# Kernel tuning notes

Hardware: AMD Instinct MI355X
Metric: run time of the kernel (lower is better)

## Reference

```python
import jax, jax.numpy as jnp
import numpy as np

D = 512       # embed_dim
H = 8         # num_heads
HD = D // H   # head_dim = 64
B = 16
TQ = 512      # query length (current segment)
TK = 1024     # key length (memory + current)
GRU_BIAS = 2.0


def _layer_norm(x, g, b, eps=1e-5):
    mu = jnp.mean(x, axis=-1, keepdims=True)
    var = jnp.mean((x - mu) ** 2, axis=-1, keepdims=True)
    return (x - mu) * jax.lax.rsqrt(var + eps) * g + b


def _gelu(x):
    # torch nn.GELU() default is the exact erf form
    return jax.nn.gelu(x, approximate=False)


def _rel_shift(x):
    # Transformer-XL relative shift. x: [B, H, Tq, Tk]
    b, h, tq, tk = x.shape
    x = jnp.pad(x, ((0, 0), (0, 0), (0, 0), (1, 0)))
    x = x.reshape(b, h, tk + 1, tq)[:, :, 1:, :]
    return x.reshape(b, h, tq, tk)


def _gru_gate(x, y, W, bg):
    # GTrXL gating: x is the residual stream, y the sublayer output.
    Wr, Ur, Wz, Uz, Wg, Ug = W
    r = jax.nn.sigmoid(y @ Wr + x @ Ur)
    z = jax.nn.sigmoid(y @ Wz + x @ Uz - bg)
    h = jnp.tanh(y @ Wg + (r * x) @ Ug)
    return (1.0 - z) * x + z * h


def setup_inputs() -> dict:
    key = jax.random.key(0)
    ks = jax.random.split(key, 16)
    s = 0.02
    return {
        "query": jax.random.normal(ks[0], (B, TQ, D), jnp.float32),
        "key": jax.random.normal(ks[1], (B, TK, D), jnp.float32),
        "pos_embedding": jax.random.normal(ks[2], (TK, D), jnp.float32),
        "U": jax.random.normal(ks[3], (H, HD), jnp.float32) * s,
        "V": jax.random.normal(ks[4], (H, HD), jnp.float32) * s,
        # attention projections: Wq, Wk, Wv, Wpos, Wout (no biases)
        "attn_W": jax.random.normal(ks[5], (5, D, D), jnp.float32) * s,
        "ln1_g": jnp.ones((D,), jnp.float32),
        "ln1_b": jnp.zeros((D,), jnp.float32),
        "ln2_g": jnp.ones((D,), jnp.float32),
        "ln2_b": jnp.zeros((D,), jnp.float32),
        # GRU gates: stacked [Wr, Ur, Wz, Uz, Wg, Ug], bias bg init to gru_bias
        "gate1_W": jax.random.normal(ks[6], (6, D, D), jnp.float32) * s,
        "gate1_b": jnp.full((D,), GRU_BIAS, jnp.float32),
        "gate2_W": jax.random.normal(ks[7], (6, D, D), jnp.float32) * s,
        "gate2_b": jnp.full((D,), GRU_BIAS, jnp.float32),
        "fc_W1": jax.random.normal(ks[8], (D, 4 * D), jnp.float32) * s,
        "fc_b1": jnp.zeros((4 * D,), jnp.float32),
        "fc_W2": jax.random.normal(ks[9], (4 * D, D), jnp.float32) * s,
        "fc_b2": jnp.zeros((D,), jnp.float32),
    }


def reference(query, key, pos_embedding, U, V, attn_W,
              ln1_g, ln1_b, ln2_g, ln2_b,
              gate1_W, gate1_b, gate2_W, gate2_b,
              fc_W1, fc_b1, fc_W2, fc_b2):
    b, tq, d = query.shape
    tk = key.shape[1]
    hd = d // H

    nq = _layer_norm(query, ln1_g, ln1_b)
    nk = _layer_norm(key, ln1_g, ln1_b)

    Wq, Wk, Wv, Wp, Wo = attn_W
    q = (nq @ Wq).reshape(b, tq, H, hd)
    k = (nk @ Wk).reshape(b, tk, H, hd)
    v = (nk @ Wv).reshape(b, tk, H, hd)
    p = (pos_embedding @ Wp).reshape(tk, H, hd)

    # Transformer-XL: content score (q+U)k^T + position score (q+V)p^T (rel-shifted)
    AC = jnp.einsum('bqhd,bkhd->bhqk', q + U, k)
    BD = _rel_shift(jnp.einsum('bqhd,khd->bhqk', q + V, p))
    scores = (AC + BD) / jnp.sqrt(jnp.asarray(hd, query.dtype))
    attn = jax.nn.softmax(scores, axis=-1)

    Y = jnp.einsum('bhqk,bkhd->bqhd', attn, v).reshape(b, tq, d) @ Wo
    Y = _gelu(Y)  # dropout = 0.0

    out = _gru_gate(query, Y, gate1_W, gate1_b)
    h2 = _layer_norm(out, ln2_g, ln2_b)
    E = _gelu(_gelu(h2 @ fc_W1 + fc_b1) @ fc_W2 + fc_b2)
    out = _gru_gate(out, E, gate2_W, gate2_b)
    return out
```

## Files before the change

kernel.cpp:

```cpp
#include <hip/hip_runtime.h>
#include <hip/hip_bf16.h>

typedef unsigned short u16;
typedef __attribute__((ext_vector_type(4))) float f4;
typedef __attribute__((ext_vector_type(8))) short s16x8;
typedef __attribute__((ext_vector_type(8))) unsigned short u16x8;
typedef __attribute__((ext_vector_type(4))) unsigned short u16x4;
typedef __attribute__((ext_vector_type(4))) int i32x4;
typedef __attribute__((ext_vector_type(2))) unsigned u32x2;

__device__ __forceinline__ u16 f2bf(float x){
  unsigned u = __float_as_uint(x);
  u += 0x7fffu + ((u >> 16) & 1u);
  return (u16)(u >> 16);
}
__device__ __forceinline__ float bf2f(u16 h){ return __uint_as_float(((unsigned)h) << 16); }

__device__ __forceinline__ unsigned cvt_pk_bf16(float lo, float hi){
  unsigned r;
  asm("v_cvt_pk_bf16_f32 %0, %1, %2" : "=v"(r) : "v"(lo), "v"(hi));
  return r;
}

__device__ __forceinline__ void gload_lds16(const u16* g, u16* l){
  __builtin_amdgcn_global_load_lds((__attribute__((address_space(1))) void*)g,
                                   (__attribute__((address_space(3))) void*)l, 16, 0, 0);
}

__device__ __forceinline__ float gelu_f(float x){
  float u = x * (0.7978845608f + 0.0356774081f * x * x);
  float e = __expf(-2.f * u);
  return x * __builtin_amdgcn_rcpf(1.f + e);
}
__device__ __forceinline__ float sig_f(float x){
  float e = __expf(-x);
  return __builtin_amdgcn_rcpf(1.f + e);
}
__device__ __forceinline__ float tanh_f(float x){
  float e = __expf(-2.f * fabsf(x));
  float t = (1.f - e) * __builtin_amdgcn_rcpf(1.f + e);
  return copysignf(t, x);
}

struct GemmP {
  const u16* A; const u16* B;
  const u16* A2; const u16* B2;
  int K1, K2, lda, ldb, H;
  long long sAb, sAh, sBb, sBh;
  u16* C; long long sCb, sCh; int ldc;
  u16* C2;
  const float* bias; const float* bias2;
  u16* S;
};

enum { EPI_BF16=0, EPI_QUV=1, EPI_SIG=2, EPI_TANH=3, EPI_GELU=4, EPI_BD=5 };

template<int BM, int BN, int EPI, int DB>
__launch_bounds__(256)
__global__ void gemm_k(GemmP p) {
  constexpr int WN = (BN >= 128) ? 2 : 1;
  constexpr int WM = 4 / WN;
  constexpr int TM = BM / WM, TN = BN / WN;
  constexpr int FM = TM / 16, FN = TN / 16;
  constexpr int BUFE = (BM + BN) * 64;

  __shared__ __align__(16) u16 lds[BUFE * (DB ? 2 : 1)];

  const int tid = threadIdx.x;
  const int w = tid >> 6, lane = tid & 63;
  const int bz = blockIdx.z;
  const int b = bz / p.H, h = bz - b * p.H;
  const int m0 = blockIdx.x * BM, n0 = blockIdx.y * BN;

  const u16* Ab0 = p.A + (long long)b * p.sAb + (long long)h * p.sAh + (long long)m0 * p.lda;
  const u16* Bb0 = p.B + (long long)b * p.sBb + (long long)h * p.sBh + (long long)n0 * p.ldb;
  const u16* Ab1 = p.A2 ? p.A2 + (long long)m0 * p.lda : (const u16*)0;
  const u16* Bb1 = p.B2 ? p.B2 + (long long)n0 * p.ldb : (const u16*)0;

  f4 acc[FM][FN];
  #pragma unroll
  for (int i = 0; i < FM; ++i)
    #pragma unroll
    for (int j = 0; j < FN; ++j) acc[i][j] = f4{0.f, 0.f, 0.f, 0.f};

  const int s1 = p.K1 >> 6;
  const int st = s1 + (p.K2 >> 6);
  const int wM = w / WN, wN = w - wM * WN;

  const int srow = tid >> 3;
  const long long sc8 = (long long)(((tid & 7) ^ (srow & 7)) << 3);
  const long long aoff = (long long)srow * p.lda + sc8;
  const long long boff = (long long)srow * p.ldb + sc8;

  auto stage = [&](int s, u16* lA_, u16* lB_) {
    const u16* Ab; const u16* Bb; int k0;
    if (s < s1) { Ab = Ab0; Bb = Bb0; k0 = s << 6; }
    else        { Ab = Ab1; Bb = Bb1; k0 = (s - s1) << 6; }
    const u16* pa = Ab + aoff + k0;
    const u16* pb = Bb + boff + k0;
    #pragma unroll
    for (int i = 0; i < (BM >> 5); ++i)
      gload_lds16(pa + (long long)(i * 32) * p.lda, lA_ + (size_t)(i * 4 + w) * 512);
    #pragma unroll
    for (int i = 0; i < (BN >> 5); ++i)
      gload_lds16(pb + (long long)(i * 32) * p.ldb, lB_ + (size_t)(i * 4 + w) * 512);
  };

  auto compute = [&](const u16* lA_, const u16* lB_) {
    #pragma unroll
    for (int kk = 0; kk < 2; ++kk) {
      const int kb = lane >> 4;
      const int gc = kk * 4 + kb;
      s16x8 av[FM], bv[FN];
      #pragma unroll
      for (int fm = 0; fm < FM; ++fm) {
        int r = wM * TM + fm * 16 + (lane & 15);
        av[fm] = *(const s16x8*)(lA_ + r * 64 + ((gc ^ (r & 7)) << 3));
      }
      #pragma unroll
      for (int fn = 0; fn < FN; ++fn) {
        int r = wN * TN + fn * 16 + (lane & 15);
        bv[fn] = *(const s16x8*)(lB_ + r * 64 + ((gc ^ (r & 7)) << 3));
      }
      #pragma unroll
      for (int fm = 0; fm < FM; ++fm)
        #pragma unroll
        for (int fn = 0; fn < FN; ++fn)
          acc[fm][fn] = __builtin_amdgcn_mfma_f32_16x16x32_bf16(av[fm], bv[fn], acc[fm][fn], 0, 0, 0);
    }
  };

  if constexpr (DB) {
    stage(0, lds, lds + BM * 64);
    __syncthreads();
    for (int s = 0; s < st; ++s) {
      u16* cur = lds + (size_t)(s & 1) * BUFE;
      if (s + 1 < st) {
        u16* nxt = lds + (size_t)((s + 1) & 1) * BUFE;
        stage(s + 1, nxt, nxt + BM * 64);
      }
      compute(cur, cur + BM * 64);
      __syncthreads();
    }
  } else {
    for (int s = 0; s < st; ++s) {
      stage(s, lds, lds + BM * 64);
      __syncthreads();
      compute(lds, lds + BM * 64);
      __syncthreads();
    }
  }

  const int rb = (lane >> 4) << 2;
  const int cb = lane & 15;

  if constexpr (EPI == EPI_BD) {
    #pragma unroll
    for (int fm = 0; fm < FM; ++fm)
      #pragma unroll
      for (int fn = 0; fn < FN; ++fn)
        #pragma unroll
        for (int r = 0; r < 4; ++r) {
          int row = m0 + wM * TM + fm * 16 + rb + r;
          int t   = n0 + wN * TN + fn * 16 + cb;
          int bb = row >> 9, q = row & 511;
          u16* Sp = p.S + (size_t)(bb * 8 + h) * 524800;
          Sp[(size_t)q * 1025 + 1 + t] = f2bf(acc[fm][fn][r] * 0.125f);
          if (t == 0 && q > 0) Sp[(size_t)q * 1025] = 0;
        }
  } else if constexpr (EPI == EPI_QUV) {
    #pragma unroll
    for (int fm = 0; fm < FM; ++fm)
      #pragma unroll
      for (int fn = 0; fn < FN; ++fn)
        #pragma unroll
        for (int r = 0; r < 4; ++r) {
          int row = m0 + wM * TM + fm * 16 + rb + r;
          int col = n0 + wN * TN + fn * 16 + cb;
          size_t o = (size_t)row * p.ldc + col;
          float x = acc[fm][fn][r];
          p.C[o]  = f2bf(x + p.bias[col]);
          p.C2[o] = f2bf(x + p.bias2[col]);
        }
  } else {
    u16* Cb = p.C + (long long)b * p.sCb + (long long)h * p.sCh;
    #pragma unroll
    for (int fm = 0; fm < FM; ++fm)
      #pragma unroll
      for (int fn = 0; fn < FN; ++fn)
        #pragma unroll
        for (int r = 0; r < 4; ++r) {
          int row = m0 + wM * TM + fm * 16 + rb + r;
          int col = n0 + wN * TN + fn * 16 + cb;
          float x = acc[fm][fn][r];
          if (p.bias) x += p.bias[col];
          if constexpr (EPI == EPI_SIG)  x = sig_f(x);
          if constexpr (EPI == EPI_TANH) x = tanh_f(x);
          if constexpr (EPI == EPI_GELU) x = gelu_f(x);
          Cb[(size_t)row * p.ldc + col] = f2bf(x);
        }
  }
}

__launch_bounds__(512)
__global__ void fattn_k(const u16* __restrict__ qU, const u16* __restrict__ kv,
                        const u16* __restrict__ vT, const u16* __restrict__ BD,
                        u16* __restrict__ Y) {
  __shared__ __align__(16) u16 sBuf[2 * 16384];

  const int tid = threadIdx.x, w = tid >> 6, lane = tid & 63;
  const int q0 = blockIdx.x * 128;
  const int bz = blockIdx.y, b = bz >> 3, h = bz & 7;
  const int cq = lane & 15, kb = lane >> 4;
  const u16* Sb = BD + (size_t)bz * 524800;

  auto stage = [&](int j0, u16* buf) {
    u16* sK_ = buf; u16* sV_ = buf + 4096; u16* sB_ = buf + 8192;
    {
      int c = tid, row = c >> 3, cc = c & 7, sc = cc ^ (row & 7);
      gload_lds16(kv + ((size_t)(b * 1024 + j0 + row)) * 1024 + h * 64 + sc * 8,
                  sK_ + (size_t)w * 512);
      gload_lds16(vT + (size_t)bz * 65536 + (size_t)row * 1024 + j0 + sc * 8,
                  sV_ + (size_t)w * 512);
    }
    #pragma unroll
    for (int i = 0; i < 2; ++i) {
      int c = i * 512 + tid, row = c >> 3, cc = c & 7, sc = cc ^ (row & 7);
      gload_lds16(Sb + 512 + (size_t)(q0 + row) * 1024 + j0 + sc * 8,
                  sB_ + (size_t)(i * 8 + w) * 512);
    }
  };

  const int qloc = w * 16 + cq;
  const u16* qrow = qU + ((size_t)(b * 512 + q0 + qloc)) * 512 + h * 64;
  s16x8 qb0 = *(const s16x8*)(qrow + kb * 8);
  s16x8 qb1 = *(const s16x8*)(qrow + 32 + kb * 8);

  stage(0, sBuf);
  __syncthreads();

  float m_s = -1e30f, l_s = 0.f;
  f4 O[4];
  #pragma unroll
  for (int fd = 0; fd < 4; ++fd) O[fd] = f4{0.f, 0.f, 0.f, 0.f};

  const int sw = qloc & 7;
  const int idxA = (cq + ((kb & 1) * 2) * 16) * 4;
  const int idxB = idxA + 64;

  for (int it = 0; it < 16; ++it) {
    u16* buf = sBuf + (size_t)(it & 1) * 16384;
    u16* sK_ = buf; u16* sV_ = buf + 4096; u16* sB_ = buf + 8192;
    if (it < 15) stage((it + 1) * 64, sBuf + (size_t)((it + 1) & 1) * 16384);

    f4 acc[4];
    #pragma unroll
    for (int fkv = 0; fkv < 4; ++fkv) acc[fkv] = f4{0.f, 0.f, 0.f, 0.f};
    #pragma unroll
    for (int fkv = 0; fkv < 4; ++fkv) {
      int r = fkv * 16 + cq;
      s16x8 a0 = *(const s16x8*)(sK_ + r * 64 + ((kb ^ (r & 7)) << 3));
      s16x8 a1 = *(const s16x8*)(sK_ + r * 64 + (((4 + kb) ^ (r & 7)) << 3));
      acc[fkv] = __builtin_amdgcn_mfma_f32_16x16x32_bf16(a0, qb0, acc[fkv], 0, 0, 0);
      acc[fkv] = __builtin_amdgcn_mfma_f32_16x16x32_bf16(a1, qb1, acc[fkv], 0, 0, 0);
    }

    float p[4][4];
    float tm = -1e30f;
    #pragma unroll
    for (int fkv = 0; fkv < 4; ++fkv) {
      int j8 = 2 * fkv + (kb >> 1);
      u16x4 bdv = *(const u16x4*)(sB_ + qloc * 64 + ((j8 ^ sw) << 3) + (kb & 1) * 4);
      #pragma unroll
      for (int r = 0; r < 4; ++r) {
        float s = acc[fkv][r] * 0.125f + bf2f(bdv[r]);
        p[fkv][r] = s;
        tm = fmaxf(tm, s);
      }
    }
    tm = fmaxf(tm, __shfl_xor(tm, 16));
    tm = fmaxf(tm, __shfl_xor(tm, 32));
    float mn = fmaxf(m_s, tm);
    float al = __expf(m_s - mn);
    m_s = mn;
    float ps = 0.f;
    #pragma unroll
    for (int fkv = 0; fkv < 4; ++fkv)
      #pragma unroll
      for (int r = 0; r < 4; ++r) { p[fkv][r] = __expf(p[fkv][r] - mn); ps += p[fkv][r]; }
    ps += __shfl_xor(ps, 16);
    ps += __shfl_xor(ps, 32);
    l_s = l_s * al + ps;
    #pragma unroll
    for (int fd = 0; fd < 4; ++fd)
      #pragma unroll
      for (int r = 0; r < 4; ++r) O[fd][r] *= al;

    unsigned W[4][2];
    #pragma unroll
    for (int fkv = 0; fkv < 4; ++fkv) {
      W[fkv][0] = cvt_pk_bf16(p[fkv][0], p[fkv][1]);
      W[fkv][1] = cvt_pk_bf16(p[fkv][2], p[fkv][3]);
    }
    s16x8 pb[2];
    #pragma unroll
    for (int c = 0; c < 2; ++c) {
      int a00 = __builtin_amdgcn_ds_bpermute(idxA, (int)W[2 * c][0]);
      int a01 = __builtin_amdgcn_ds_bpermute(idxA, (int)W[2 * c][1]);
      int a10 = __builtin_amdgcn_ds_bpermute(idxA, (int)W[2 * c + 1][0]);
      int a11 = __builtin_amdgcn_ds_bpermute(idxA, (int)W[2 * c + 1][1]);
      int b00 = __builtin_amdgcn_ds_bpermute(idxB, (int)W[2 * c][0]);
      int b01 = __builtin_amdgcn_ds_bpermute(idxB, (int)W[2 * c][1]);
      int b10 = __builtin_amdgcn_ds_bpermute(idxB, (int)W[2 * c + 1][0]);
      int b11 = __builtin_amdgcn_ds_bpermute(idxB, (int)W[2 * c + 1][1]);
      bool hi = (kb >= 2);
      i32x4 t;
      t[0] = hi ? a10 : a00;
      t[1] = hi ? a11 : a01;
      t[2] = hi ? b10 : b00;
      t[3] = hi ? b11 : b01;
      pb[c] = *(s16x8*)&t;
    }

    #pragma unroll
    for (int c = 0; c < 2; ++c)
      #pragma unroll
      for (int fd = 0; fd < 4; ++fd) {
        int rd = fd * 16 + cq;
        s16x8 vb = *(const s16x8*)(sV_ + rd * 64 + (((c * 4 + kb) ^ (rd & 7)) << 3));
        O[fd] = __builtin_amdgcn_mfma_f32_16x16x32_bf16(vb, pb[c], O[fd], 0, 0, 0);
      }
    __syncthreads();
  }

  float invl = 1.f / l_s;
  u16* yrow = Y + ((size_t)(b * 512 + q0 + qloc)) * 512 + h * 64;
  #pragma unroll
  for (int fd = 0; fd < 4; ++fd) {
    unsigned w0 = cvt_pk_bf16(O[fd][0] * invl, O[fd][1] * invl);
    unsigned w1 = cvt_pk_bf16(O[fd][2] * invl, O[fd][3] * invl);
    u32x2 st; st[0] = w0; st[1] = w1;
    *(u32x2*)(yrow + fd * 16 + kb * 4) = st;
  }
}

__launch_bounds__(256)
__global__ void ln_k(const float* __restrict__ x, const float* __restrict__ g,
                     const float* __restrict__ be, u16* __restrict__ out) {
  int row  = blockIdx.x * 4 + (threadIdx.x >> 6);
  int lane = threadIdx.x & 63;
  const float* xr = x + (size_t)row * 512 + lane * 8;
  f4 v0 = *(const f4*)xr;
  f4 v1 = *(const f4*)(xr + 4);
  float s = 0.f, q = 0.f;
  #pragma unroll
  for (int i = 0; i < 4; ++i) { s += v0[i] + v1[i]; q += v0[i]*v0[i] + v1[i]*v1[i]; }
  #pragma unroll
  for (int o = 32; o > 0; o >>= 1) { s += __shfl_xor(s, o); q += __shfl_xor(q, o); }
  float mu = s * (1.f / 512.f);
  float rs = rsqrtf(q * (1.f / 512.f) - mu * mu + 1e-5f);
  int c = lane * 8;
  u16x8 o;
  #pragma unroll
  for (int i = 0; i < 8; ++i) {
    float xx = (i < 4) ? v0[i] : v1[i - 4];
    o[i] = f2bf((xx - mu) * rs * g[c + i] + be[c + i]);
  }
  *(u16x8*)(out + (size_t)row * 512 + c) = o;
}

__device__ __forceinline__ void tbody(float (*t)[65], const float* src, u16* dst,
                                      int R, int C, int bx, int by, int tid) {
  int c0 = bx * 64, r0 = by * 64;
  #pragma unroll
  for (int i = 0; i < 4; ++i) {
    int r = i * 16 + (tid >> 4);
    int c4 = (tid & 15) * 4;
    f4 v = *(const f4*)(src + (size_t)(r0 + r) * C + c0 + c4);
    t[r][c4] = v.x; t[r][c4 + 1] = v.y; t[r][c4 + 2] = v.z; t[r][c4 + 3] = v.w;
  }
  __syncthreads();
  #pragma unroll
  for (int i = 0; i < 2; ++i) {
    int id = i * 256 + tid;
    int rr = id >> 3, c8 = (id & 7) * 8;
    u16x8 o;
    #pragma unroll
    for (int j = 0; j < 8; ++j) o[j] = f2bf(t[c8 + j][rr]);
    *(u16x8*)(dst + (size_t)(c0 + rr) * R + r0 + c8) = o;
  }
}

__launch_bounds__(256)
__global__ void tsq_k(const float* aW, const float* g1W, const float* g2W, u16* wT) {
  __shared__ float t[64][65];
  int z = blockIdx.z;
  const int lut[6] = {0, 2, 1, 3, 4, 5};
  const float* src; u16* dst;
  if (z < 5)       { src = aW  + (size_t)z * 262144;        dst = wT + (size_t)z * 262144; }
  else if (z < 11) { int j = z - 5;  src = g1W + (size_t)j * 262144; dst = wT + (size_t)(5 + lut[j]) * 262144; }
  else             { int j = z - 11; src = g2W + (size_t)j * 262144; dst = wT + (size_t)(11 + lut[j]) * 262144; }
  tbody(t, src, dst, 512, 512, blockIdx.x, blockIdx.y, threadIdx.x);
}

__launch_bounds__(256)
__global__ void tgen_k(const float* src, u16* dst, int R, int C) {
  __shared__ float t[64][65];
  tbody(t, src, dst, R, C, blockIdx.x, blockIdx.y, threadIdx.x);
}

__launch_bounds__(256)
__global__ void vtrans_k(const u16* kv, u16* vT) {
  int jt = blockIdx.x, h = blockIdx.y, b = blockIdx.z;
  __shared__ u16 t[64][72];
  int tid = threadIdx.x;
  const u16* src = kv + ((size_t)b * 1024 + jt * 64) * 1024 + 512 + h * 64;
  #pragma unroll
  for (int i = 0; i < 2; ++i) {
    int id = i * 256 + tid;
    int r = id >> 3, c = (id & 7) * 8;
    u16x8 v = *(const u16x8*)(src + (size_t)r * 1024 + c);
    #pragma unroll
    for (int j = 0; j < 8; ++j) t[r][c + j] = v[j];
  }
  __syncthreads();
  u16* dst = vT + (size_t)(b * 8 + h) * 65536 + (size_t)jt * 64;
  #pragma unroll
  for (int i = 0; i < 2; ++i) {
    int id = i * 256 + tid;
    int d = id >> 3, c = (id & 7) * 8;
    u16x8 o;
    #pragma unroll
    for (int j = 0; j < 8; ++j) o[j] = t[c + j][d];
    *(u16x8*)(dst + (size_t)d * 1024 + c) = o;
  }
}

__launch_bounds__(256)
__global__ void conv_k(const float* in, u16* out, int n8) {
  int i = blockIdx.x * 256 + threadIdx.x;
  if (i >= n8) return;
  const float* p = in + (size_t)i * 8;
  f4 a = *(const f4*)p, b = *(const f4*)(p + 4);
  u16x8 o;
  #pragma unroll
  for (int j = 0; j < 4; ++j) { o[j] = f2bf(a[j]); o[4 + j] = f2bf(b[j]); }
  *(u16x8*)(out + (size_t)i * 8) = o;
}

__launch_bounds__(256)
__global__ void bias_k(const float* g1b, const float* g2b, float* b1, float* b2) {
  int i = blockIdx.x * 256 + threadIdx.x;
  if (i < 1024) { b1[i] = (i < 512) ? 0.f : -g1b[i - 512]; b2[i] = (i < 512) ? 0.f : -g2b[i - 512]; }
}

__launch_bounds__(256)
__global__ void rx_k(const u16* rz, const float* x, u16* rx) {
  int i = blockIdx.x * 256 + threadIdx.x;
  int m = i >> 6, d8 = (i & 63) << 3;
  u16x8 rv = *(const u16x8*)(rz + (size_t)m * 1024 + d8);
  const float* xp = x + (size_t)m * 512 + d8;
  f4 x0 = *(const f4*)xp, x1 = *(const f4*)(xp + 4);
  u16x8 o;
  #pragma unroll
  for (int j = 0; j < 4; ++j) { o[j] = f2bf(bf2f(rv[j]) * x0[j]); o[4 + j] = f2bf(bf2f(rv[4 + j]) * x1[j]); }
  *(u16x8*)(rx + (size_t)m * 512 + d8) = o;
}

__launch_bounds__(256)
__global__ void comb_k(const u16* rz, const u16* hg, const float* x, float* of, u16* ob) {
  int i = blockIdx.x * 256 + threadIdx.x;
  int m = i >> 6, d8 = (i & 63) << 3;
  u16x8 zv = *(const u16x8*)(rz + (size_t)m * 1024 + 512 + d8);
  u16x8 hv = *(const u16x8*)(hg + (size_t)m * 512 + d8);
  const float* xp = x + (size_t)m * 512 + d8;
  f4 x0 = *(const f4*)xp, x1 = *(const f4*)(xp + 4);
  f4 o0, o1; u16x8 obv;
  #pragma unroll
  for (int j = 0; j < 4; ++j) {
    float z = bf2f(zv[j]), hh = bf2f(hv[j]);
    float r = (1.f - z) * x0[j] + z * hh; o0[j] = r; obv[j] = f2bf(r);
  }
  #pragma unroll
  for (int j = 0; j < 4; ++j) {
    float z = bf2f(zv[4 + j]), hh = bf2f(hv[4 + j]);
    float r = (1.f - z) * x1[j] + z * hh; o1[j] = r; obv[4 + j] = f2bf(r);
  }
  float* op = of + (size_t)m * 512 + d8;
  *(f4*)op = o0; *(f4*)(op + 4) = o1;
  if (ob) *(u16x8*)(ob + (size_t)m * 512 + d8) = obv;
}

extern "C" void kernel_launch(void* const* d_in, const int* in_sizes, int n_in,
                              void* d_out, int out_size, void* d_ws, size_t ws_size,
                              hipStream_t stream) {
  const float* query = (const float*)d_in[0];
  const float* key   = (const float*)d_in[1];
  const float* pos   = (const float*)d_in[2];
  const float* U     = (const float*)d_in[3];
  const float* V     = (const float*)d_in[4];
  const float* attnW = (const float*)d_in[5];
  const float* ln1g  = (const float*)d_in[6];
  const float* ln1b  = (const float*)d_in[7];
  const float* ln2g  = (const float*)d_in[8];
  const float* ln2b  = (const float*)d_in[9];
  const float* g1W   = (const float*)d_in[10];
  const float* g1b   = (const float*)d_in[11];
  const float* g2W   = (const float*)d_in[12];
  const float* g2b   = (const float*)d_in[13];
  const float* fcW1  = (const float*)d_in[14];
  const float* fcb1  = (const float*)d_in[15];
  const float* fcW2  = (const float*)d_in[16];
  const float* fcb2  = (const float*)d_in[17];
  float* outp = (float*)d_out;

  char* base = (char*)d_ws;
  size_t off = 0;
  auto alloc = [&](size_t bytes) -> char* {
    char* p = base + off;
    off += (bytes + 255) & ~(size_t)255;
    return p;
  };

  u16* wT     = (u16*)alloc(17ull * 262144 * 2);
  u16* fc1T   = (u16*)alloc(2048ull * 512 * 2);
  u16* fc2T   = (u16*)alloc(2048ull * 512 * 2);
  u16* posb   = (u16*)alloc(1024ull * 512 * 2);
  u16* pbf    = (u16*)alloc(1024ull * 512 * 2);
  float* bias1 = (float*)alloc(1024 * 4);
  float* bias2 = (float*)alloc(1024 * 4);
  u16* nq     = (u16*)alloc(8192ull * 512 * 2);
  u16* nk     = (u16*)alloc(16384ull * 512 * 2);
  u16* xq     = (u16*)alloc(8192ull * 512 * 2);
  u16* qU     = (u16*)alloc(8192ull * 512 * 2);
  u16* qV     = (u16*)alloc(8192ull * 512 * 2);
  u16* kv     = (u16*)alloc(16384ull * 1024 * 2);
  u16* y1     = (u16*)alloc(8192ull * 512 * 2);
  u16* ob1    = (u16*)alloc(8192ull * 512 * 2);
  u16* S      = (u16*)alloc(128ull * 524800 * 2 + 4096);
  if (off > ws_size) return;

  u16* Y = nq;
  u16* vT = nk;
  float* out1f = (float*)qU;
  u16* rz1 = S;
  u16* rx1 = S + 8388608;
  u16* hg1 = rx1 + 4194304;
  u16* h2  = hg1 + 4194304;
  u16* e1  = h2 + 4194304;
  u16* y2  = e1 + 16777216;
  u16* rz2 = y2 + 4194304;
  u16* rx2 = rz2 + 8388608;
  u16* hg2 = rx2 + 4194304;

  bias_k<<<dim3(4), dim3(256), 0, stream>>>(g1b, g2b, bias1, bias2);
  tsq_k<<<dim3(8, 8, 17), dim3(256), 0, stream>>>(attnW, g1W, g2W, wT);
  tgen_k<<<dim3(32, 8), dim3(256), 0, stream>>>(fcW1, fc1T, 512, 2048);
  tgen_k<<<dim3(8, 32), dim3(256), 0, stream>>>(fcW2, fc2T, 2048, 512);
  conv_k<<<dim3(256), dim3(256), 0, stream>>>(pos, posb, 65536);
  conv_k<<<dim3(2048), dim3(256), 0, stream>>>(query, xq, 524288);
  ln_k<<<dim3(2048), dim3(256), 0, stream>>>(query, ln1g, ln1b, nq);
  ln_k<<<dim3(4096), dim3(256), 0, stream>>>(key, ln1g, ln1b, nk);

  { GemmP p{}; p.A = nq; p.B = wT; p.K1 = 512; p.lda = 512; p.ldb = 512; p.H = 1;
    p.C = qU; p.C2 = qV; p.ldc = 512; p.bias = U; p.bias2 = V;
    gemm_k<64,128,EPI_QUV,1><<<dim3(128,4,1), dim3(256), 0, stream>>>(p); }
  { GemmP p{}; p.A = nk; p.B = wT + 1ull*262144; p.K1 = 512; p.lda = 512; p.ldb = 512; p.H = 1;
    p.C = kv; p.ldc = 1024;
    gemm_k<64,128,EPI_BF16,1><<<dim3(256,8,1), dim3(256), 0, stream>>>(p); }
  { GemmP p{}; p.A = posb; p.B = wT + 3ull*262144; p.K1 = 512; p.lda = 512; p.ldb = 512; p.H = 1;
    p.C = pbf; p.ldc = 512;
    gemm_k<64,128,EPI_BF16,1><<<dim3(16,4,1), dim3(256), 0, stream>>>(p); }
  vtrans_k<<<dim3(16, 8, 16), dim3(256), 0, stream>>>(kv, vT);

  { GemmP p{}; p.A = qV; p.lda = 512; p.sAh = 64;
    p.B = pbf; p.ldb = 512; p.sBh = 64; p.K1 = 64; p.H = 8; p.S = S;
    gemm_k<128,128,EPI_BD,0><<<dim3(64,8,8), dim3(256), 0, stream>>>(p); }

  fattn_k<<<dim3(4, 128), dim3(512), 0, stream>>>(qU, kv, vT, S, Y);

  { GemmP p{}; p.A = Y; p.B = wT + 4ull*262144; p.K1 = 512; p.lda = 512; p.ldb = 512; p.H = 1;
    p.C = y1; p.ldc = 512;
    gemm_k<64,128,EPI_GELU,1><<<dim3(128,4,1), dim3(256), 0, stream>>>(p); }

  { GemmP p{}; p.A = y1; p.B = wT + 5ull*262144; p.K1 = 512;
    p.A2 = xq; p.B2 = wT + 7ull*262144; p.K2 = 512;
    p.lda = 512; p.ldb = 512; p.H = 1; p.C = rz1; p.ldc = 1024; p.bias = bias1;
    gemm_k<64,128,EPI_SIG,1><<<dim3(128,8,1), dim3(256), 0, stream>>>(p); }
  rx_k<<<dim3(2048), dim3(256), 0, stream>>>(rz1, query, rx1);
  { GemmP p{}; p.A = y1; p.B = wT + 9ull*262144; p.K1 = 512;
    p.A2 = rx1; p.B2 = wT + 10ull*262144; p.K2 = 512;
    p.lda = 512; p.ldb = 512; p.H = 1; p.C = hg1; p.ldc = 512;
    gemm_k<64,128,EPI_TANH,1><<<dim3(128,4,1), dim3(256), 0, stream>>>(p); }
  comb_k<<<dim3(2048), dim3(256), 0, stream>>>(rz1, hg1, query, out1f, ob1);

  ln_k<<<dim3(2048), dim3(256), 0, stream>>>(out1f, ln2g, ln2b, h2);
  { GemmP p{}; p.A = h2; p.B = fc1T; p.K1 = 512; p.lda = 512; p.ldb = 512; p.H = 1;
    p.C = e1; p.ldc = 2048; p.bias = fcb1;
    gemm_k<64,128,EPI_GELU,1><<<dim3(128,16,1), dim3(256), 0, stream>>>(p); }
  { GemmP p{}; p.A = e1; p.B = fc2T; p.K1 = 2048; p.lda = 2048; p.ldb = 2048; p.H = 1;
    p.C = y2; p.ldc = 512; p.bias = fcb2;
    gemm_k<64,128,EPI_GELU,1><<<dim3(128,4,1), dim3(256), 0, stream>>>(p); }

  { GemmP p{}; p.A = y2; p.B = wT + 11ull*262144; p.K1 = 512;
    p.A2 = ob1; p.B2 = wT + 13ull*262144; p.K2 = 512;
    p.lda = 512; p.ldb = 512; p.H = 1; p.C = rz2; p.ldc = 1024; p.bias = bias2;
    gemm_k<64,128,EPI_SIG,1><<<dim3(128,8,1), dim3(256), 0, stream>>>(p); }
  rx_k<<<dim3(2048), dim3(256), 0, stream>>>(rz2, out1f, rx2);
  { GemmP p{}; p.A = y2; p.B = wT + 15ull*262144; p.K1 = 512;
    p.A2 = rx2; p.B2 = wT + 16ull*262144; p.K2 = 512;
    p.lda = 512; p.ldb = 512; p.H = 1; p.C = hg2; p.ldc = 512;
    gemm_k<64,128,EPI_TANH,1><<<dim3(128,4,1), dim3(256), 0, stream>>>(p); }
  comb_k<<<dim3(2048), dim3(256), 0, stream>>>(rz2, hg2, out1f, outp, (u16*)nullptr);
}
```

Before: 400.3 us.

## Fuse V transpose into KV projection epilogue and triple-buffer attention loads

The K/V projection GEMM now writes K in row-major form and V already transposed per head, so the separate vtrans kernel and its extra pass over V go away. The flash attention kernel now triple-buffers K/V tiles and double-buffers the BD tiles. It waits with explicit vmcnt counts and a raw barrier instead of a full __syncthreads, so loads stay in flight across iterations. The FC1 GEMM switches to a new three-buffer prefetch mode. The cost is more LDS per block, which may lower occupancy, and hand-written waitcnt logic that must match the exact number of loads issued.

New measurement: 424.5 us. 6.0% more time.

```diff
diff --git a/kernel.cpp b/kernel.cpp
--- a/kernel.cpp
+++ b/kernel.cpp
@@ -26,6 +26,10 @@
   __builtin_amdgcn_global_load_lds((__attribute__((address_space(1))) void*)g,
                                    (__attribute__((address_space(3))) void*)l, 16, 0, 0);
 }
+
+__device__ __forceinline__ void vm_wait0(){ asm volatile("s_waitcnt vmcnt(0)" ::: "memory"); }
+__device__ __forceinline__ void vm_wait2(){ asm volatile("s_waitcnt vmcnt(2)" ::: "memory"); }
+__device__ __forceinline__ void vm_wait6(){ asm volatile("s_waitcnt vmcnt(6)" ::: "memory"); }
 
 __device__ __forceinline__ float gelu_f(float x){
   float u = x * (0.7978845608f + 0.0356774081f * x * x);
@@ -53,7 +57,7 @@
   u16* S;
 };
 
-enum { EPI_BF16=0, EPI_QUV=1, EPI_SIG=2, EPI_TANH=3, EPI_GELU=4, EPI_BD=5 };
+enum { EPI_BF16=0, EPI_QUV=1, EPI_SIG=2, EPI_TANH=3, EPI_GELU=4, EPI_BD=5, EPI_KVT=6 };
 
 template<int BM, int BN, int EPI, int DB>
 __launch_bounds__(256)
@@ -63,8 +67,9 @@
   constexpr int TM = BM / WM, TN = BN / WN;
   constexpr int FM = TM / 16, FN = TN / 16;
   constexpr int BUFE = (BM + BN) * 64;
-
-  __shared__ __align__(16) u16 lds[BUFE * (DB ? 2 : 1)];
+  constexpr int NBUF = (DB == 2) ? 3 : (DB == 1) ? 2 : 1;
+
+  __shared__ __align__(16) u16 lds[BUFE * NBUF];
 
   const int tid = threadIdx.x;
   const int w = tid >> 6, lane = tid & 63;
@@ -130,7 +135,21 @@
     }
   };
 
-  if constexpr (DB) {
+  if constexpr (DB == 2) {
+    stage(0, lds, lds + BM * 64);
+    stage(1, lds + BUFE, lds + BUFE + BM * 64);
+    for (int s = 0; s < st; ++s) {
+      if (s + 1 < st) vm_wait6(); else vm_wait0();
+      __builtin_amdgcn_s_barrier();
+      __builtin_amdgcn_sched_barrier(0);
+      u16* cur = lds + (size_t)(s % 3) * BUFE;
+      if (s + 2 < st) {
+        u16* nxt = lds + (size_t)((s + 2) % 3) * BUFE;
+        stage(s + 2, nxt, nxt + BM * 64);
+      }
+      compute(cur, cur + BM * 64);
+    }
+  } else if constexpr (DB == 1) {
     stage(0, lds, lds + BM * 64);
     __syncthreads();
     for (int s = 0; s < st; ++s) {
@@ -168,6 +187,32 @@
           Sp[(size_t)q * 1025 + 1 + t] = f2bf(acc[fm][fn][r] * 0.125f);
           if (t == 0 && q > 0) Sp[(size_t)q * 1025] = 0;
         }
+  } else if constexpr (EPI == EPI_KVT) {
+    if (n0 < 512) {
+      #pragma unroll
+      for (int fm = 0; fm < FM; ++fm)
+        #pragma unroll
+        for (int fn = 0; fn < FN; ++fn)
+          #pragma unroll
+          for (int r = 0; r < 4; ++r) {
+            int row = m0 + wM * TM + fm * 16 + rb + r;
+            int col = n0 + wN * TN + fn * 16 + cb;
+            p.C[(size_t)row * 512 + col] = f2bf(acc[fm][fn][r]);
+          }
+    } else {
+      #pragma unroll
+      for (int fm = 0; fm < FM; ++fm)
+        #pragma unroll
+        for (int fn = 0; fn < FN; ++fn) {
+          int j0r = m0 + wM * TM + fm * 16 + rb;
+          int d   = n0 - 512 + wN * TN + fn * 16 + cb;
+          int bb = j0r >> 10, j = j0r & 1023;
+          u16x4 v;
+          #pragma unroll
+          for (int r = 0; r < 4; ++r) v[r] = f2bf(acc[fm][fn][r]);
+          *(u16x4*)(p.C2 + (((size_t)(bb * 8 + (d >> 6))) << 16) + (size_t)(d & 63) * 1024 + j) = v;
+        }
+    }
   } else if constexpr (EPI == EPI_QUV) {
     #pragma unroll
     for (int fm = 0; fm < FM; ++fm)
@@ -203,10 +248,10 @@
 }
 
 __launch_bounds__(512)
-__global__ void fattn_k(const u16* __restrict__ qU, const u16* __restrict__ kv,
+__global__ void fattn_k(const u16* __restrict__ qU, const u16* __restrict__ kvK,
                         const u16* __restrict__ vT, const u16* __restrict__ BD,
                         u16* __restrict__ Y) {
-  __shared__ __align__(16) u16 sBuf[2 * 16384];
+  __shared__ __align__(16) u16 sBuf[3 * 8192 + 2 * 8192];
 
   const int tid = threadIdx.x, w = tid >> 6, lane = tid & 63;
   const int q0 = blockIdx.x * 128;
@@ -214,20 +259,19 @@
   const int cq = lane & 15, kb = lane >> 4;
   const u16* Sb = BD + (size_t)bz * 524800;
 
-  auto stage = [&](int j0, u16* buf) {
-    u16* sK_ = buf; u16* sV_ = buf + 4096; u16* sB_ = buf + 8192;
-    {
-      int c = tid, row = c >> 3, cc = c & 7, sc = cc ^ (row & 7);
-      gload_lds16(kv + ((size_t)(b * 1024 + j0 + row)) * 1024 + h * 64 + sc * 8,
-                  sK_ + (size_t)w * 512);
-      gload_lds16(vT + (size_t)bz * 65536 + (size_t)row * 1024 + j0 + sc * 8,
-                  sV_ + (size_t)w * 512);
-    }
+  auto stageKV = [&](int j0, u16* buf) {
+    int row = tid >> 3, sc = (tid & 7) ^ (row & 7);
+    gload_lds16(kvK + ((size_t)(b * 1024 + j0 + row)) * 512 + h * 64 + sc * 8,
+                buf + (size_t)w * 512);
+    gload_lds16(vT + (size_t)bz * 65536 + (size_t)row * 1024 + j0 + sc * 8,
+                buf + 4096 + (size_t)w * 512);
+  };
+  auto stageBD = [&](int j0, u16* buf) {
     #pragma unroll
     for (int i = 0; i < 2; ++i) {
-      int c = i * 512 + tid, row = c >> 3, cc = c & 7, sc = cc ^ (row & 7);
+      int c = i * 512 + tid, row = c >> 3, sc = (c & 7) ^ (row & 7);
       gload_lds16(Sb + 512 + (size_t)(q0 + row) * 1024 + j0 + sc * 8,
-                  sB_ + (size_t)(i * 8 + w) * 512);
+                  buf + (size_t)(i * 8 + w) * 512);
     }
   };
 
@@ -236,8 +280,9 @@
   s16x8 qb0 = *(const s16x8*)(qrow + kb * 8);
   s16x8 qb1 = *(const s16x8*)(qrow + 32 + kb * 8);
 
-  stage(0, sBuf);
-  __syncthreads();
+  stageKV(0, sBuf);
+  stageBD(0, sBuf + 24576);
+  stageKV(64, sBuf + 8192);
 
   float m_s = -1e30f, l_s = 0.f;
   f4 O[4];
@@ -249,9 +294,16 @@
   const int idxB = idxA + 64;
 
   for (int it = 0; it < 16; ++it) {
-    u16* buf = sBuf + (size_t)(it & 1) * 16384;
-    u16* sK_ = buf; u16* sV_ = buf + 4096; u16* sB_ = buf + 8192;
-    if (it < 15) stage((it + 1) * 64, sBuf + (size_t)((it + 1) & 1) * 16384);
+    if (it < 15) vm_wait2(); else vm_wait0();
+    __builtin_amdgcn_s_barrier();
+    __builtin_amdgcn_sched_barrier(0);
+
+    u16* kvb = sBuf + (size_t)(it % 3) * 8192;
+    u16* sK_ = kvb; u16* sV_ = kvb + 4096;
+    u16* sB_ = sBuf + 24576 + (size_t)(it & 1) * 8192;
+
+    if (it + 1 < 16) stageBD((it + 1) * 64, sBuf + 24576 + (size_t)((it + 1) & 1) * 8192);
+    if (it + 2 < 16) stageKV((it + 2) * 64, sBuf + (size_t)((it + 2) % 3) * 8192);
 
     f4 acc[4];
     #pragma unroll
@@ -330,7 +382,6 @@
         s16x8 vb = *(const s16x8*)(sV_ + rd * 64 + (((c * 4 + kb) ^ (rd & 7)) << 3));
         O[fd] = __builtin_amdgcn_mfma_f32_16x16x32_bf16(vb, pb[c], O[fd], 0, 0, 0);
       }
-    __syncthreads();
   }
 
   float invl = 1.f / l_s;
@@ -407,33 +458,6 @@
 __global__ void tgen_k(const float* src, u16* dst, int R, int C) {
   __shared__ float t[64][65];
   tbody(t, src, dst, R, C, blockIdx.x, blockIdx.y, threadIdx.x);
-}
-
-__launch_bounds__(256)
-__global__ void vtrans_k(const u16* kv, u16* vT) {
-  int jt = blockIdx.x, h = blockIdx.y, b = blockIdx.z;
-  __shared__ u16 t[64][72];
-  int tid = threadIdx.x;
-  const u16* src = kv + ((size_t)b * 1024 + jt * 64) * 1024 + 512 + h * 64;
-  #pragma unroll
-  for (int i = 0; i < 2; ++i) {
-    int id = i * 256 + tid;
-    int r = id >> 3, c = (id & 7) * 8;
-    u16x8 v = *(const u16x8*)(src + (size_t)r * 1024 + c);
-    #pragma unroll
-    for (int j = 0; j < 8; ++j) t[r][c + j] = v[j];
-  }
-  __syncthreads();
-  u16* dst = vT + (size_t)(b * 8 + h) * 65536 + (size_t)jt * 64;
-  #pragma unroll
-  for (int i = 0; i < 2; ++i) {
-    int id = i * 256 + tid;
-    int d = id >> 3, c = (id & 7) * 8;
-    u16x8 o;
-    #pragma unroll
-    for (int j = 0; j < 8; ++j) o[j] = t[c + j][d];
-    *(u16x8*)(dst + (size_t)d * 1024 + c) = o;
-  }
 }
 
 __launch_bounds__(256)
@@ -534,14 +558,14 @@
   u16* xq     = (u16*)alloc(8192ull * 512 * 2);
   u16* qU     = (u16*)alloc(8192ull * 512 * 2);
   u16* qV     = (u16*)alloc(8192ull * 512 * 2);
-  u16* kv     = (u16*)alloc(16384ull * 1024 * 2);
+  u16* kvK    = (u16*)alloc(16384ull * 512 * 2);
+  u16* vT     = (u16*)alloc(128ull * 65536 * 2);
   u16* y1     = (u16*)alloc(8192ull * 512 * 2);
   u16* ob1    = (u16*)alloc(8192ull * 512 * 2);
   u16* S      = (u16*)alloc(128ull * 524800 * 2 + 4096);
   if (off > ws_size) return;
 
   u16* Y = nq;
-  u16* vT = nk;
   float* out1f = (float*)qU;
   u16* rz1 = S;
   u16* rx1 = S + 8388608;
@@ -566,18 +590,17 @@
     p.C = qU; p.C2 = qV; p.ldc = 512; p.bias = U; p.bias2 = V;
     gemm_k<64,128,EPI_QUV,1><<<dim3(128,4,1), dim3(256), 0, stream>>>(p); }
   { GemmP p{}; p.A = nk; p.B = wT + 1ull*262144; p.K1 = 512; p.lda = 512; p.ldb = 512; p.H = 1;
-    p.C = kv; p.ldc = 1024;
-    gemm_k<64,128,EPI_BF16,1><<<dim3(256,8,1), dim3(256), 0, stream>>>(p); }
+    p.C = kvK; p.C2 = vT; p.ldc = 512;
+    gemm_k<64,128,EPI_KVT,1><<<dim3(256,8,1), dim3(256), 0, stream>>>(p); }
   { GemmP p{}; p.A = posb; p.B = wT + 3ull*262144; p.K1 = 512; p.lda = 512; p.ldb = 512; p.H = 1;
     p.C = pbf; p.ldc = 512;
     gemm_k<64,128,EPI_BF16,1><<<dim3(16,4,1), dim3(256), 0, stream>>>(p); }
-  vtrans_k<<<dim3(16, 8, 16), dim3(256), 0, stream>>>(kv, vT);
 
   { GemmP p{}; p.A = qV; p.lda = 512; p.sAh = 64;
     p.B = pbf; p.ldb = 512; p.sBh = 64; p.K1 = 64; p.H = 8; p.S = S;
     gemm_k<128,128,EPI_BD,0><<<dim3(64,8,8), dim3(256), 0, stream>>>(p); }
 
-  fattn_k<<<dim3(4, 128), dim3(512), 0, stream>>>(qU, kv, vT, S, Y);
+  fattn_k<<<dim3(4, 128), dim3(512), 0, stream>>>(qU, kvK, vT, S, Y);
 
   { GemmP p{}; p.A = Y; p.B = wT + 4ull*262144; p.K1 = 512; p.lda = 512; p.ldb = 512; p.H = 1;
     p.C = y1; p.ldc = 512;
@@ -597,7 +620,7 @@
   ln_k<<<dim3(2048), dim3(256), 0, stream>>>(out1f, ln2g, ln2b, h2);
   { GemmP p{}; p.A = h2; p.B = fc1T; p.K1 = 512; p.lda = 512; p.ldb = 512; p.H = 1;
     p.C = e1; p.ldc = 2048; p.bias = fcb1;
-    gemm_k<64,128,EPI_GELU,1><<<dim3(128,16,1), dim3(256), 0, stream>>>(p); }
+    gemm_k<64,128,EPI_GELU,2><<<dim3(128,16,1), dim3(256), 0, stream>>>(p); }
   { GemmP p{}; p.A = e1; p.B = fc2T; p.K1 = 2048; p.lda = 2048; p.ldb = 2048; p.H = 1;
     p.C = y2; p.ldc = 512; p.bias = fcb2;
     gemm_k<64,128,EPI_GELU,1><<<dim3(128,4,1), dim3(256), 0, stream>>>(p); }
```

## Triple-buffer K/V and double-buffer BD in flash attention with vmcnt waits

Applied to the files above, without the earlier changes.

Restructures the attention kernel's LDS staging. K/V tiles are now triple-buffered and prefetched two iterations ahead, while the BD tile stays double-buffered one iteration ahead. The end-of-loop __syncthreads is replaced by explicit s_waitcnt vmcnt plus s_barrier at the top of each iteration, so global loads can stay in flight across iterations. It also raises wave priority around the MFMA blocks. LDS use grows, which may lower occupancy, and correctness depends on the hand-counted vmcnt values matching the number of outstanding loads.

After: 400.7 us. About the same (+0.1%).

```diff
diff --git a/kernel.cpp b/kernel.cpp
--- a/kernel.cpp
+++ b/kernel.cpp
@@ -26,6 +26,9 @@
   __builtin_amdgcn_global_load_lds((__attribute__((address_space(1))) void*)g,
                                    (__attribute__((address_space(3))) void*)l, 16, 0, 0);
 }
+
+__device__ __forceinline__ void vm_wait0(){ asm volatile("s_waitcnt vmcnt(0)" ::: "memory"); }
+__device__ __forceinline__ void vm_wait2(){ asm volatile("s_waitcnt vmcnt(2)" ::: "memory"); }
 
 __device__ __forceinline__ float gelu_f(float x){
   float u = x * (0.7978845608f + 0.0356774081f * x * x);
@@ -206,7 +209,7 @@
 __global__ void fattn_k(const u16* __restrict__ qU, const u16* __restrict__ kv,
                         const u16* __restrict__ vT, const u16* __restrict__ BD,
                         u16* __restrict__ Y) {
-  __shared__ __align__(16) u16 sBuf[2 * 16384];
+  __shared__ __align__(16) u16 sBuf[3 * 8192 + 2 * 8192];
 
   const int tid = threadIdx.x, w = tid >> 6, lane = tid & 63;
   const int q0 = blockIdx.x * 128;
@@ -214,20 +217,19 @@
   const int cq = lane & 15, kb = lane >> 4;
   const u16* Sb = BD + (size_t)bz * 524800;
 
-  auto stage = [&](int j0, u16* buf) {
-    u16* sK_ = buf; u16* sV_ = buf + 4096; u16* sB_ = buf + 8192;
-    {
-      int c = tid, row = c >> 3, cc = c & 7, sc = cc ^ (row & 7);
-      gload_lds16(kv + ((size_t)(b * 1024 + j0 + row)) * 1024 + h * 64 + sc * 8,
-                  sK_ + (size_t)w * 512);
-      gload_lds16(vT + (size_t)bz * 65536 + (size_t)row * 1024 + j0 + sc * 8,
-                  sV_ + (size_t)w * 512);
-    }
+  auto stageKV = [&](int j0, u16* buf) {
+    int row = tid >> 3, sc = (tid & 7) ^ (row & 7);
+    gload_lds16(kv + ((size_t)(b * 1024 + j0 + row)) * 1024 + h * 64 + sc * 8,
+                buf + (size_t)w * 512);
+    gload_lds16(vT + (size_t)bz * 65536 + (size_t)row * 1024 + j0 + sc * 8,
+                buf + 4096 + (size_t)w * 512);
+  };
+  auto stageBD = [&](int j0, u16* buf) {
     #pragma unroll
     for (int i = 0; i < 2; ++i) {
-      int c = i * 512 + tid, row = c >> 3, cc = c & 7, sc = cc ^ (row & 7);
+      int c = i * 512 + tid, row = c >> 3, sc = (c & 7) ^ (row & 7);
       gload_lds16(Sb + 512 + (size_t)(q0 + row) * 1024 + j0 + sc * 8,
-                  sB_ + (size_t)(i * 8 + w) * 512);
+                  buf + (size_t)(i * 8 + w) * 512);
     }
   };
 
@@ -236,8 +238,9 @@
   s16x8 qb0 = *(const s16x8*)(qrow + kb * 8);
   s16x8 qb1 = *(const s16x8*)(qrow + 32 + kb * 8);
 
-  stage(0, sBuf);
-  __syncthreads();
+  stageKV(0, sBuf);
+  stageBD(0, sBuf + 24576);
+  stageKV(64, sBuf + 8192);
 
   float m_s = -1e30f, l_s = 0.f;
   f4 O[4];
@@ -249,13 +252,21 @@
   const int idxB = idxA + 64;
 
   for (int it = 0; it < 16; ++it) {
-    u16* buf = sBuf + (size_t)(it & 1) * 16384;
-    u16* sK_ = buf; u16* sV_ = buf + 4096; u16* sB_ = buf + 8192;
-    if (it < 15) stage((it + 1) * 64, sBuf + (size_t)((it + 1) & 1) * 16384);
+    if (it < 15) vm_wait2(); else vm_wait0();
+    __builtin_amdgcn_s_barrier();
+    __builtin_amdgcn_sched_barrier(0);
+
+    u16* kvb = sBuf + (size_t)(it % 3) * 8192;
+    u16* sK_ = kvb; u16* sV_ = kvb + 4096;
+    u16* sB_ = sBuf + 24576 + (size_t)(it & 1) * 8192;
+
+    if (it + 1 < 16) stageBD((it + 1) * 64, sBuf + 24576 + (size_t)((it + 1) & 1) * 8192);
+    if (it + 2 < 16) stageKV((it + 2) * 64, sBuf + (size_t)((it + 2) % 3) * 8192);
 
     f4 acc[4];
     #pragma unroll
     for (int fkv = 0; fkv < 4; ++fkv) acc[fkv] = f4{0.f, 0.f, 0.f, 0.f};
+    __builtin_amdgcn_s_setprio(1);
     #pragma unroll
     for (int fkv = 0; fkv < 4; ++fkv) {
       int r = fkv * 16 + cq;
@@ -264,6 +275,7 @@
       acc[fkv] = __builtin_amdgcn_mfma_f32_16x16x32_bf16(a0, qb0, acc[fkv], 0, 0, 0);
       acc[fkv] = __builtin_amdgcn_mfma_f32_16x16x32_bf16(a1, qb1, acc[fkv], 0, 0, 0);
     }
+    __builtin_amdgcn_s_setprio(0);
 
     float p[4][4];
     float tm = -1e30f;
@@ -322,6 +334,7 @@
       pb[c] = *(s16x8*)&t;
     }
 
+    __builtin_amdgcn_s_setprio(1);
     #pragma unroll
     for (int c = 0; c < 2; ++c)
       #pragma unroll
@@ -330,7 +343,7 @@
         s16x8 vb = *(const s16x8*)(sV_ + rd * 64 + (((c * 4 + kb) ^ (rd & 7)) << 3));
         O[fd] = __builtin_amdgcn_mfma_f32_16x16x32_bf16(vb, pb[c], O[fd], 0, 0, 0);
       }
-    __syncthreads();
+    __builtin_amdgcn_s_setprio(0);
   }
 
   float invl = 1.f / l_s;
```
